# Kernel tuning notes

Hardware: AMD Instinct MI355X
Metric: run time of the kernel (lower is better)

Reference implementation:

```python
import jax, jax.numpy as jnp
import numpy as np

B, C, H, W = 2, 256, 96, 96
CQ = C // 8  # q/k channel dim = 32


def setup_inputs() -> dict:
    key = jax.random.key(0)
    k1, k2, k3 = jax.random.split(key, 3)
    x = jax.random.normal(k1, (B, C, H, W), dtype=jnp.float32)
    # 1x1 conv weight [out=2*C/8+C, in=C] (spectral_norm is a weight
    # parametrization; post-normalization the forward is a plain 1x1 conv,
    # so we treat w as the already-normalized weight). Scaled ~ unit sigma.
    w = jax.random.normal(k2, (2 * CQ + C, C), dtype=jnp.float32) * 0.05
    gamma = jax.random.normal(k3, (1,), dtype=jnp.float32)
    return {"x": x, "w": w, "gamma": gamma}


def reference(x, w, gamma):
    b, c, h, wd = x.shape
    n = h * wd
    xf = x.reshape(b, c, n)                      # [B, C, N]
    qkv = jnp.einsum('oc,bcn->bon', w, xf)       # 1x1 conv == channel matmul
    q = qkv[:, :CQ]                              # [B, C/8, N]
    k = qkv[:, CQ:2 * CQ]                        # [B, C/8, N]
    v = qkv[:, 2 * CQ:]                          # [B, C,   N]
    scores = jnp.einsum('bdi,bdj->bij', q, k)    # [B, N, N] = q^T k
    attn = jax.nn.softmax(scores, axis=1)        # softmax over i (dim=1)
    o = jnp.einsum('bci,bij->bcj', v, attn)      # [B, C, N]
    return (gamma * o).reshape(b, c, h, wd) + x
```

## Files before the change

kernel.cpp:

```cpp
#include <hip/hip_runtime.h>
#include <hip/hip_bf16.h>

#define NTOK 9216
#define CCH  256
#define DQK  32
#define BJ   128
#define BI   64
#define SSEG 8
#define SI   72

typedef __attribute__((ext_vector_type(8))) short short8;
typedef __attribute__((ext_vector_type(4))) float f32x4;

__device__ __forceinline__ unsigned short f2bf(float x) {
    union { float f; unsigned int u; } v; v.f = x;
    return (unsigned short)((v.u + 0x7FFF + ((v.u >> 16) & 1)) >> 16);
}
__device__ __forceinline__ float bf2f(unsigned short h) {
    union { unsigned int u; float f; } v; v.u = ((unsigned int)h) << 16; return v.f;
}

#if __has_builtin(__builtin_amdgcn_cvt_pk_bf16_f32)
__device__ __forceinline__ unsigned int pack2bf(float a, float b) {
    auto p = __builtin_amdgcn_cvt_pk_bf16_f32(a, b);
    union { decltype(p) v; unsigned int u; } cv; cv.v = p; return cv.u;
}
#else
__device__ __forceinline__ unsigned int pack2bf(float a, float b) {
    return (unsigned)f2bf(a) | ((unsigned)f2bf(b) << 16);
}
#endif

#if __has_builtin(__builtin_amdgcn_exp2f)
#define EXP2(x) __builtin_amdgcn_exp2f(x)
#else
#define EXP2(x) __expf((x) * 0.69314718055994531f)
#endif

__global__ __launch_bounds__(256) void wcvt_kernel(
    const float* __restrict__ w, unsigned short* __restrict__ wbf)
{
    const int i = (blockIdx.x * 256 + threadIdx.x) * 4;
    f32x4 v = *(const f32x4*)(w + i);
    *(unsigned int*)(wbf + i)     = pack2bf(v[0], v[1]);
    *(unsigned int*)(wbf + i + 2) = pack2bf(v[2], v[3]);
}

__global__ __launch_bounds__(256) void qkv_kernel(
    const float* __restrict__ x, const unsigned short* __restrict__ wbf,
    unsigned short* __restrict__ qT, unsigned short* __restrict__ kT,
    unsigned short* __restrict__ vcn)
{
    const int id   = blockIdx.x;
    const int b    = id & 1;
    const int n0   = (id >> 1) * 16;
    const int t    = threadIdx.x;
    const int wv   = t >> 6;
    const int lane = t & 63;
    const int l15  = lane & 15;
    const int qd   = lane >> 4;

    const float* xb = x + (size_t)b * CCH * NTOK + n0 + l15;

    f32x4 acc[5];
#pragma unroll
    for (int tt = 0; tt < 5; ++tt) acc[tt] = (f32x4){0.f, 0.f, 0.f, 0.f};

    const unsigned short* wrow = wbf + (size_t)(80 * wv + l15) * CCH + qd * 8;

#pragma unroll
    for (int kk = 0; kk < 8; ++kk) {
        float xe[8];
#pragma unroll
        for (int e = 0; e < 8; ++e)
            xe[e] = xb[(size_t)(32 * kk + 8 * qd + e) * NTOK];
        short8 bfr;
#pragma unroll
        for (int e = 0; e < 8; ++e)
            bfr[e] = (short)f2bf(xe[e]);
#pragma unroll
        for (int tt = 0; tt < 5; ++tt) {
            short8 afr = *(const short8*)(wrow + (size_t)(16 * tt) * CCH + 32 * kk);
            acc[tt] = __builtin_amdgcn_mfma_f32_16x16x32_bf16(afr, bfr, acc[tt], 0, 0, 0);
        }
    }

    const int n = n0 + l15;
    const float L2E = 1.44269504088896f;
#pragma unroll
    for (int tt = 0; tt < 5; ++tt) {
        const int o0l = 80 * wv + 16 * tt + 4 * qd;
        if (o0l < 32) {
            unsigned short* d = qT + ((size_t)b * NTOK + n) * DQK + o0l;
            *(unsigned int*)d       = pack2bf(acc[tt][0] * L2E, acc[tt][1] * L2E);
            *(unsigned int*)(d + 2) = pack2bf(acc[tt][2] * L2E, acc[tt][3] * L2E);
        } else if (o0l < 64) {
            unsigned short* d = kT + ((size_t)b * NTOK + n) * DQK + (o0l - 32);
            *(unsigned int*)d       = pack2bf(acc[tt][0], acc[tt][1]);
            *(unsigned int*)(d + 2) = pack2bf(acc[tt][2], acc[tt][3]);
        } else {
            unsigned short* d = vcn + ((size_t)b * CCH + (o0l - 64)) * NTOK + n;
            d[0] = f2bf(acc[tt][0]);
            d[(size_t)NTOK] = f2bf(acc[tt][1]);
            d[(size_t)2 * NTOK] = f2bf(acc[tt][2]);
            d[(size_t)3 * NTOK] = f2bf(acc[tt][3]);
        }
    }
}

__global__ __launch_bounds__(256, 3) void attn_partial_kernel(
    const unsigned short* __restrict__ qT, const unsigned short* __restrict__ kT,
    const unsigned short* __restrict__ vcn,
    unsigned short* __restrict__ Opart, float* __restrict__ lpart)
{
    __shared__ __align__(16) unsigned short Pl[BJ * SI];
    __shared__ float lred2[2 * BJ];

    const int id    = blockIdx.x;
    const int combo = id & 15;
    const int s     = combo >> 1;
    const int cb    = combo & 1;
    const int r     = id >> 4;
    const int jb    = r % 72;
    const int b     = r / 72;

    const int t    = threadIdx.x;
    const int wv   = t >> 6;
    const int lane = t & 63;
    const int l15  = lane & 15;
    const int qd   = lane >> 4;
    const int jh   = wv >> 1;
    const int u    = wv & 1;
    const int j0   = jb * BJ;
    const int c0   = cb * 128;
    const int iBeg = s * (NTOK / SSEG);
    const int iEnd = iBeg + (NTOK / SSEG);

    short8 kf[4];
#pragma unroll
    for (int jt = 0; jt < 4; ++jt)
        kf[jt] = *(const short8*)(kT +
            ((size_t)b * NTOK + j0 + 64 * jh + 16 * jt + l15) * DQK + qd * 8);

    f32x4 acc[4][4];
#pragma unroll
    for (int mt = 0; mt < 4; ++mt)
#pragma unroll
        for (int ct = 0; ct < 4; ++ct)
            acc[mt][ct] = (f32x4){0.f, 0.f, 0.f, 0.f};
    float lw[4] = {0.f, 0.f, 0.f, 0.f};

    const unsigned short* qrow =
        qT + (size_t)b * NTOK * DQK + (size_t)(16 * u + l15) * DQK + qd * 8;
    const unsigned short* vrow =
        vcn + ((size_t)b * CCH + c0 + 64 * u + l15) * NTOK + qd * 8;

    for (int i0 = iBeg; i0 < iEnd; i0 += BI) {
        short8 af[2];
#pragma unroll
        for (int it = 0; it < 2; ++it)
            af[it] = *(const short8*)(qrow + (size_t)(i0 + 32 * it) * DQK);
        short8 vf[2][4];
#pragma unroll
        for (int kc = 0; kc < 2; ++kc)
#pragma unroll
            for (int ct = 0; ct < 4; ++ct)
                vf[kc][ct] = *(const short8*)(vrow + (size_t)(16 * ct) * NTOK + i0 + 32 * kc);

#pragma unroll
        for (int it = 0; it < 2; ++it) {
#pragma unroll
            for (int jt = 0; jt < 4; ++jt) {
                f32x4 sc = __builtin_amdgcn_mfma_f32_16x16x32_bf16(
                    af[it], kf[jt], (f32x4){0.f, 0.f, 0.f, 0.f}, 0, 0, 0);
                float p0 = EXP2(sc[0]);
                float p1 = EXP2(sc[1]);
                float p2 = EXP2(sc[2]);
                float p3 = EXP2(sc[3]);
                lw[jt] += (p0 + p1) + (p2 + p3);
                int base = (64 * jh + 16 * jt + l15) * SI + 32 * it + 16 * u + 4 * qd;
                *(unsigned long long*)(Pl + base) =
                    (unsigned long long)pack2bf(p0, p1) |
                    ((unsigned long long)pack2bf(p2, p3) << 32);
            }
        }
        __syncthreads();

#pragma unroll
        for (int kc = 0; kc < 2; ++kc) {
            short8 pa[4];
#pragma unroll
            for (int mt = 0; mt < 4; ++mt)
                pa[mt] = *(const short8*)(Pl + (64 * jh + 16 * mt + l15) * SI + 32 * kc + qd * 8);
#pragma unroll
            for (int mt = 0; mt < 4; ++mt)
#pragma unroll
                for (int ct = 0; ct < 4; ++ct)
                    acc[mt][ct] = __builtin_amdgcn_mfma_f32_16x16x32_bf16(
                        pa[mt], vf[kc][ct], acc[mt][ct], 0, 0, 0);
        }
        __syncthreads();
    }

#pragma unroll
    for (int jt = 0; jt < 4; ++jt) {
        lw[jt] += __shfl_xor(lw[jt], 16);
        lw[jt] += __shfl_xor(lw[jt], 32);
    }
    if (qd == 0) {
#pragma unroll
        for (int jt = 0; jt < 4; ++jt)
            lred2[u * BJ + 64 * jh + 16 * jt + l15] = lw[jt];
    }
    __syncthreads();
    if (cb == 0 && t < BJ)
        lpart[(size_t)(s * 2 + b) * NTOK + j0 + t] = lred2[t] + lred2[BJ + t];

#pragma unroll
    for (int mt = 0; mt < 4; ++mt)
#pragma unroll
        for (int ct = 0; ct < 4; ++ct) {
            int c = c0 + 64 * u + 16 * ct + l15;
            int j = j0 + 64 * jh + 16 * mt + 4 * qd;
            unsigned short* p = Opart + ((size_t)(s * 2 + b) * CCH + c) * NTOK + j;
            *(unsigned long long*)p =
                (unsigned long long)pack2bf(acc[mt][ct][0], acc[mt][ct][1]) |
                ((unsigned long long)pack2bf(acc[mt][ct][2], acc[mt][ct][3]) << 32);
        }
}

__global__ __launch_bounds__(256) void reduce_kernel(
    const unsigned short* __restrict__ Opart, const float* __restrict__ lpart,
    const float* __restrict__ x, const float* __restrict__ gamma,
    float* __restrict__ out)
{
    const size_t flat = ((size_t)blockIdx.x * 256 + threadIdx.x) * 4;
    const int j = (int)(flat % NTOK);
    const int b = (int)(flat / ((size_t)CCH * NTOK));
    const size_t inb = flat - (size_t)b * CCH * NTOK;

    f32x4 o = {0.f, 0.f, 0.f, 0.f};
    f32x4 l = {0.f, 0.f, 0.f, 0.f};
#pragma unroll
    for (int s = 0; s < SSEG; ++s) {
        const size_t plane = (size_t)(s * 2 + b) * CCH * NTOK;
        unsigned long long ov = *(const unsigned long long*)(Opart + plane + inb);
        f32x4 lv = *(const f32x4*)(lpart + (size_t)(s * 2 + b) * NTOK + j);
        o[0] += bf2f((unsigned short)(ov));
        o[1] += bf2f((unsigned short)(ov >> 16));
        o[2] += bf2f((unsigned short)(ov >> 32));
        o[3] += bf2f((unsigned short)(ov >> 48));
        l[0] += lv[0]; l[1] += lv[1]; l[2] += lv[2]; l[3] += lv[3];
    }
    const float g = gamma[0];
    f32x4 xv = *(const f32x4*)(x + flat);
    f32x4 rr;
    rr[0] = g * o[0] / l[0] + xv[0];
    rr[1] = g * o[1] / l[1] + xv[1];
    rr[2] = g * o[2] / l[2] + xv[2];
    rr[3] = g * o[3] / l[3] + xv[3];
    *(f32x4*)(out + flat) = rr;
}

extern "C" void kernel_launch(void* const* d_in, const int* in_sizes, int n_in,
                              void* d_out, int out_size, void* d_ws, size_t ws_size,
                              hipStream_t stream) {
    const float* x     = (const float*)d_in[0];
    const float* w     = (const float*)d_in[1];
    const float* gamma = (const float*)d_in[2];
    float* out = (float*)d_out;

    unsigned short* qT  = (unsigned short*)d_ws;
    unsigned short* kT  = qT + (size_t)2 * NTOK * DQK;
    unsigned short* vcn = kT + (size_t)2 * NTOK * DQK;
    unsigned short* Opart = vcn + (size_t)2 * CCH * NTOK;
    float* lpart = (float*)(Opart + (size_t)SSEG * 2 * CCH * NTOK);
    unsigned short* wbf = (unsigned short*)(lpart + (size_t)SSEG * 2 * NTOK);

    wcvt_kernel<<<80, 256, 0, stream>>>(w, wbf);

    qkv_kernel<<<1152, 256, 0, stream>>>(x, wbf, qT, kT, vcn);

    attn_partial_kernel<<<2304, 256, 0, stream>>>(qT, kT, vcn, Opart, lpart);

    reduce_kernel<<<(unsigned)((size_t)2 * CCH * NTOK / 4 / 256), 256, 0, stream>>>(
        Opart, lpart, x, gamma, out);
}
```

Baseline: 301.3 us.

## Make attention waves independent with per-wave P tiles and no block barriers

Restructures the attention partial kernel so each wavefront owns a full job (64 columns by 128 channels) with its own private shared-memory P tile, removing all __syncthreads in the inner loop and the cross-wave l reduction. Each wave computes more output tiles (4x8 accumulators) over 32-token steps, and the grid is halved with occupancy hint lowered to 2 blocks. This eliminates barrier stalls but raises register pressure, recomputes scores per channel half, and makes the key loads less shared across waves.

```diff
diff --git a/kernel.cpp b/kernel.cpp
--- a/kernel.cpp
+++ b/kernel.cpp
@@ -4,10 +4,8 @@
 #define NTOK 9216
 #define CCH  256
 #define DQK  32
-#define BJ   128
-#define BI   64
 #define SSEG 8
-#define SI   72
+#define SI2  40
 
 typedef __attribute__((ext_vector_type(8))) short short8;
 typedef __attribute__((ext_vector_type(4))) float f32x4;
@@ -108,64 +106,60 @@
     }
 }
 
-__global__ __launch_bounds__(256, 3) void attn_partial_kernel(
+__global__ __launch_bounds__(256, 2) void attn_partial_kernel(
     const unsigned short* __restrict__ qT, const unsigned short* __restrict__ kT,
     const unsigned short* __restrict__ vcn,
     unsigned short* __restrict__ Opart, float* __restrict__ lpart)
 {
-    __shared__ __align__(16) unsigned short Pl[BJ * SI];
-    __shared__ float lred2[2 * BJ];
-
-    const int id    = blockIdx.x;
-    const int combo = id & 15;
-    const int s     = combo >> 1;
-    const int cb    = combo & 1;
-    const int r     = id >> 4;
-    const int jb    = r % 72;
-    const int b     = r / 72;
-
+    __shared__ __align__(16) unsigned short Plw[4][64 * SI2];
+
+    const int id   = blockIdx.x;
     const int t    = threadIdx.x;
     const int wv   = t >> 6;
     const int lane = t & 63;
     const int l15  = lane & 15;
     const int qd   = lane >> 4;
-    const int jh   = wv >> 1;
-    const int u    = wv & 1;
-    const int j0   = jb * BJ;
+
+    const int seg  = id & 7;
+    const int job  = (id >> 3) * 4 + wv;
+    const int cb   = job & 1;
+    const int b    = (job >> 1) & 1;
+    const int jb   = job >> 2;
+    const int j0   = jb * 64;
     const int c0   = cb * 128;
-    const int iBeg = s * (NTOK / SSEG);
+    const int iBeg = seg * (NTOK / SSEG);
     const int iEnd = iBeg + (NTOK / SSEG);
+
+    unsigned short* Pw = &Plw[wv][0];
 
     short8 kf[4];
 #pragma unroll
     for (int jt = 0; jt < 4; ++jt)
         kf[jt] = *(const short8*)(kT +
-            ((size_t)b * NTOK + j0 + 64 * jh + 16 * jt + l15) * DQK + qd * 8);
-
-    f32x4 acc[4][4];
+            ((size_t)b * NTOK + j0 + 16 * jt + l15) * DQK + qd * 8);
+
+    f32x4 acc[4][8];
 #pragma unroll
     for (int mt = 0; mt < 4; ++mt)
 #pragma unroll
-        for (int ct = 0; ct < 4; ++ct)
+        for (int ct = 0; ct < 8; ++ct)
             acc[mt][ct] = (f32x4){0.f, 0.f, 0.f, 0.f};
     float lw[4] = {0.f, 0.f, 0.f, 0.f};
 
-    const unsigned short* qrow =
-        qT + (size_t)b * NTOK * DQK + (size_t)(16 * u + l15) * DQK + qd * 8;
-    const unsigned short* vrow =
-        vcn + ((size_t)b * CCH + c0 + 64 * u + l15) * NTOK + qd * 8;
-
-    for (int i0 = iBeg; i0 < iEnd; i0 += BI) {
+    const unsigned short* qbase =
+        qT + (size_t)b * NTOK * DQK + (size_t)l15 * DQK + qd * 8;
+    const unsigned short* vbase =
+        vcn + ((size_t)b * CCH + c0 + l15) * NTOK + qd * 8;
+
+    for (int i0 = iBeg; i0 < iEnd; i0 += 32) {
         short8 af[2];
 #pragma unroll
         for (int it = 0; it < 2; ++it)
-            af[it] = *(const short8*)(qrow + (size_t)(i0 + 32 * it) * DQK);
-        short8 vf[2][4];
-#pragma unroll
-        for (int kc = 0; kc < 2; ++kc)
-#pragma unroll
-            for (int ct = 0; ct < 4; ++ct)
-                vf[kc][ct] = *(const short8*)(vrow + (size_t)(16 * ct) * NTOK + i0 + 32 * kc);
+            af[it] = *(const short8*)(qbase + (size_t)(i0 + 16 * it) * DQK);
+        short8 vf[8];
+#pragma unroll
+        for (int ct = 0; ct < 8; ++ct)
+            vf[ct] = *(const short8*)(vbase + (size_t)(16 * ct) * NTOK + i0);
 
 #pragma unroll
         for (int it = 0; it < 2; ++it) {
@@ -178,28 +172,24 @@
                 float p2 = EXP2(sc[2]);
                 float p3 = EXP2(sc[3]);
                 lw[jt] += (p0 + p1) + (p2 + p3);
-                int base = (64 * jh + 16 * jt + l15) * SI + 32 * it + 16 * u + 4 * qd;
-                *(unsigned long long*)(Pl + base) =
+                int base = (16 * jt + l15) * SI2 + 16 * it + 4 * qd;
+                *(unsigned long long*)(Pw + base) =
                     (unsigned long long)pack2bf(p0, p1) |
                     ((unsigned long long)pack2bf(p2, p3) << 32);
             }
         }
-        __syncthreads();
-
-#pragma unroll
-        for (int kc = 0; kc < 2; ++kc) {
-            short8 pa[4];
-#pragma unroll
-            for (int mt = 0; mt < 4; ++mt)
-                pa[mt] = *(const short8*)(Pl + (64 * jh + 16 * mt + l15) * SI + 32 * kc + qd * 8);
-#pragma unroll
-            for (int mt = 0; mt < 4; ++mt)
-#pragma unroll
-                for (int ct = 0; ct < 4; ++ct)
-                    acc[mt][ct] = __builtin_amdgcn_mfma_f32_16x16x32_bf16(
-                        pa[mt], vf[kc][ct], acc[mt][ct], 0, 0, 0);
-        }
-        __syncthreads();
+
+        short8 pa[4];
+#pragma unroll
+        for (int mt = 0; mt < 4; ++mt)
+            pa[mt] = *(const short8*)(Pw + (16 * mt + l15) * SI2 + qd * 8);
+
+#pragma unroll
+        for (int mt = 0; mt < 4; ++mt)
+#pragma unroll
+            for (int ct = 0; ct < 8; ++ct)
+                acc[mt][ct] = __builtin_amdgcn_mfma_f32_16x16x32_bf16(
+                    pa[mt], vf[ct], acc[mt][ct], 0, 0, 0);
     }
 
 #pragma unroll
@@ -207,22 +197,19 @@
         lw[jt] += __shfl_xor(lw[jt], 16);
         lw[jt] += __shfl_xor(lw[jt], 32);
     }
-    if (qd == 0) {
+    if (cb == 0 && qd == 0) {
 #pragma unroll
         for (int jt = 0; jt < 4; ++jt)
-            lred2[u * BJ + 64 * jh + 16 * jt + l15] = lw[jt];
-    }
-    __syncthreads();
-    if (cb == 0 && t < BJ)
-        lpart[(size_t)(s * 2 + b) * NTOK + j0 + t] = lred2[t] + lred2[BJ + t];
+            lpart[(size_t)(seg * 2 + b) * NTOK + j0 + 16 * jt + l15] = lw[jt];
+    }
 
 #pragma unroll
     for (int mt = 0; mt < 4; ++mt)
 #pragma unroll
-        for (int ct = 0; ct < 4; ++ct) {
-            int c = c0 + 64 * u + 16 * ct + l15;
-            int j = j0 + 64 * jh + 16 * mt + 4 * qd;
-            unsigned short* p = Opart + ((size_t)(s * 2 + b) * CCH + c) * NTOK + j;
+        for (int ct = 0; ct < 8; ++ct) {
+            int c = c0 + 16 * ct + l15;
+            int j = j0 + 16 * mt + 4 * qd;
+            unsigned short* p = Opart + ((size_t)(seg * 2 + b) * CCH + c) * NTOK + j;
             *(unsigned long long*)p =
                 (unsigned long long)pack2bf(acc[mt][ct][0], acc[mt][ct][1]) |
                 ((unsigned long long)pack2bf(acc[mt][ct][2], acc[mt][ct][3]) << 32);
@@ -281,7 +268,7 @@
 
     qkv_kernel<<<1152, 256, 0, stream>>>(x, wbf, qT, kT, vcn);
 
-    attn_partial_kernel<<<2304, 256, 0, stream>>>(qT, kT, vcn, Opart, lpart);
+    attn_partial_kernel<<<1152, 256, 0, stream>>>(qT, kT, vcn, Opart, lpart);
 
     reduce_kernel<<<(unsigned)((size_t)2 * CCH * NTOK / 4 / 256), 256, 0, stream>>>(
         Opart, lpart, x, gamma, out);
```

Result: slower. 314.2 us (+4.3%).
